# Kernel optimization log

Hardware: AMD Instinct MI355X
Metric: run time of the kernel (lower is better)

Reference implementation:

```python
import jax, jax.numpy as jnp
import numpy as np

EPS = 1e-5

def _ln(x, g, b):
    m = jnp.mean(x, axis=-1, keepdims=True)
    v = jnp.var(x, axis=-1, keepdims=True)
    return (x - m) / jnp.sqrt(v + EPS) * g + b

def setup_inputs() -> dict:
    key = jax.random.key(0)
    ks = jax.random.split(key, 16)
    B, T, N, K, d, E = 2, 12, 512, 8, 64, 64
    D = K * d
    s = 0.02
    inp = {
        "x": jax.random.normal(ks[0], (B, T, N, D), jnp.float32),
        "lapmatrix": jax.random.normal(ks[1], (N, N), jnp.float32),
        "node_embeddings": jax.random.normal(ks[2], (N, E), jnp.float32),
        "Wq": jax.random.normal(ks[3], (D, D), jnp.float32) * s,
        "bq": jnp.zeros((D,), jnp.float32),
        "Wk": jax.random.normal(ks[4], (D, D), jnp.float32) * s,
        "bk": jnp.zeros((D,), jnp.float32),
        "Wv": jax.random.normal(ks[5], (D, D), jnp.float32) * s,
        "bv": jnp.zeros((D,), jnp.float32),
        "Wo": jax.random.normal(ks[6], (D, D), jnp.float32) * s,
        "bo": jnp.zeros((D,), jnp.float32),
        "W1": jax.random.normal(ks[7], (4 * D, D), jnp.float32) * s,
        "b1": jnp.zeros((4 * D,), jnp.float32),
        "W2": jax.random.normal(ks[8], (D, 4 * D), jnp.float32) * s,
        "b2": jnp.zeros((D,), jnp.float32),
        "g1": jnp.ones((D,), jnp.float32),
        "be1": jnp.zeros((D,), jnp.float32),
        "g2": jnp.ones((D,), jnp.float32),
        "be2": jnp.zeros((D,), jnp.float32),
        "alpha": jnp.float32(1.0),
        "beta": jnp.float32(1.0),
        "k": 3,
    }
    return inp

def reference(x, lapmatrix, node_embeddings, Wq, bq, Wk, bk, Wv, bv, Wo, bo,
              W1, b1, W2, b2, g1, be1, g2, be2, alpha, beta, k):
    B, T, N, D = x.shape
    K, d = 8, D // 8
    x_raw = x
    xn = _ln(x, g1, be1)
    q = (xn @ Wq.T + bq).reshape(B, T, N, K, d)
    kk = (xn @ Wk.T + bk).reshape(B, T, N, K, d)
    v = (xn @ Wv.T + bv).reshape(B, T, N, K, d)
    # raw attention logits: [B,T,K,N,N]
    raw = jnp.einsum('btnkd,btmkd->btknm', q, kk) / jnp.sqrt(jnp.float32(d))
    # graph biases, all [N,N], broadcast over B,T,K
    supports = jax.nn.softmax(jax.nn.relu(node_embeddings @ node_embeddings.T), axis=1)
    adj = (lapmatrix != 0).astype(x.dtype)
    mask = jnp.where(adj == 0, jnp.float32(-1e9), jnp.float32(0.0))
    logits = raw + alpha * supports + beta * lapmatrix + mask
    attn = jax.nn.softmax(logits, axis=-1)  # dropout = identity in eval
    out = jnp.einsum('btknm,btmkd->btnkd', attn, v).reshape(B, T, N, D)
    x1 = x_raw + (out @ Wo.T + bo)
    h = _ln(x1, g2, be2)
    ffn = jax.nn.relu(h @ W1.T + b1) @ W2.T + b2
    return x1 + ffn
```

## Files before the change

### kernel.cpp

```cpp
#include <hip/hip_runtime.h>

typedef unsigned short u16;
typedef unsigned int   u32;
typedef __attribute__((ext_vector_type(8))) short bf16x8;
typedef __attribute__((ext_vector_type(4))) float f32x4;

#define DEV static __device__ __forceinline__

DEV float b2f(u16 u){ return __uint_as_float(((u32)u)<<16); }
DEV u16 f2b(float f){
  u32 u = __float_as_uint(f);
  u32 r = (u + 0x7FFFu + ((u>>16)&1u)) >> 16;
  return (u16)r;
}

union V8 { uint4 v; u16 s[8]; };

DEV u32 cvt_pk_bf16(float lo, float hi){
  u32 r;
  asm("v_cvt_pk_bf16_f32 %0, %1, %2" : "=v"(r) : "v"(lo), "v"(hi));
  return r;
}

DEV bool is_f32(const void* dt){ return *(const u32*)dt == 0x3F800000u; }

DEV uint4 ld8_ext_bf(const void* p, size_t i, bool f32){
  if(f32){
    const float* q = (const float*)p + i;
    float4 a = *(const float4*)q, b = *(const float4*)(q+4);
    V8 r;
    r.s[0]=f2b(a.x); r.s[1]=f2b(a.y); r.s[2]=f2b(a.z); r.s[3]=f2b(a.w);
    r.s[4]=f2b(b.x); r.s[5]=f2b(b.y); r.s[6]=f2b(b.z); r.s[7]=f2b(b.w);
    return r.v;
  }
  return *(const uint4*)((const u16*)p + i);
}
DEV void ld8_ext_f(const void* p, size_t i, bool f32, float* o){
  if(f32){
    const float* q = (const float*)p + i;
    float4 a = *(const float4*)q, b = *(const float4*)(q+4);
    o[0]=a.x;o[1]=a.y;o[2]=a.z;o[3]=a.w;o[4]=b.x;o[5]=b.y;o[6]=b.z;o[7]=b.w;
  }else{
    V8 u; u.v = *(const uint4*)((const u16*)p + i);
    #pragma unroll
    for(int k=0;k<8;k++) o[k]=b2f(u.s[k]);
  }
}
DEV float ld1_ext(const void* p, size_t i, bool f32){
  return f32 ? ((const float*)p)[i] : b2f(((const u16*)p)[i]);
}
DEV float load_scalar(const void* p, bool f32){
  return f32 ? *(const float*)p : b2f(*(const u16*)p);
}

DEV void gl_lds16(const u16* g, u16* l){
  __builtin_amdgcn_global_load_lds((const __attribute__((address_space(1))) void*)g,
                                   (__attribute__((address_space(3))) void*)l, 16, 0, 0);
}

__global__ __launch_bounds__(256) void sentinel_kernel(u16* out, long n, const void* dt){
  long ne = is_f32(dt) ? 2*n : n;
  long i = (long)blockIdx.x*256 + threadIdx.x;
  if(i < ne) out[i] = 0x4442;
}

__global__ __launch_bounds__(256) void prep_kernel(
    const void* __restrict__ x, const void* __restrict__ g1,
    const void* __restrict__ be1, u16* __restrict__ xn,
    const void* Wq, const void* Wk, const void* Wv, const void* Wo,
    const void* W1, const void* W2, u16* __restrict__ wbf,
    const void* bq, const void* bk, const void* bv, const void* bo,
    const void* b1, const void* b2, float* __restrict__ bfp,
    const void* __restrict__ E, const void* __restrict__ lap,
    const void* __restrict__ alpha_p, const void* __restrict__ beta_p,
    float* __restrict__ bm, const void* dt)
{
  __shared__ float En[64];
  __shared__ float red[8];
  const bool f32 = is_f32(dt);
  const int bid = blockIdx.x, t = threadIdx.x;

  if(bid < 3072){
    const int row = bid*4 + (t>>6), lane = t&63;
    float v[8];
    ld8_ext_f(x, (size_t)row*512 + lane*8, f32, v);
    float s=0.f, ss=0.f;
    #pragma unroll
    for(int i=0;i<8;i++){ s+=v[i]; ss+=v[i]*v[i]; }
    #pragma unroll
    for(int o=1;o<64;o<<=1){ s+=__shfl_xor(s,o,64); ss+=__shfl_xor(ss,o,64); }
    const float mean = s*(1.0f/512.0f);
    const float var  = ss*(1.0f/512.0f) - mean*mean;
    const float rstd = rsqrtf(var + 1e-5f);
    float gv[8], bv[8];
    ld8_ext_f(g1, (size_t)lane*8, f32, gv);
    ld8_ext_f(be1, (size_t)lane*8, f32, bv);
    V8 o8;
    #pragma unroll
    for(int i=0;i<8;i++) o8.s[i]=f2b((v[i]-mean)*rstd*gv[i]+bv[i]);
    *(uint4*)(xn+(size_t)row*512+lane*8)=o8.v;
  } else if(bid < 4608){
    size_t i = ((size_t)(bid-3072)*256 + t)*8;
    const void* src; size_t base;
    if(i < 262144){ src=Wq; base=0; }
    else if(i < 524288){ src=Wk; base=262144; }
    else if(i < 786432){ src=Wv; base=524288; }
    else if(i < 1048576){ src=Wo; base=786432; }
    else if(i < 2097152){ src=W1; base=1048576; }
    else { src=W2; base=2097152; }
    *(uint4*)(wbf + i) = ld8_ext_bf(src, i-base, f32);
  } else if(bid < 5120){
    const int n = bid - 4608;
    if(t < 64) En[t] = ld1_ext(E, (size_t)n*64 + t, f32);
    __syncthreads();
    const float alpha = load_scalar(alpha_p, f32);
    const float beta  = load_scalar(beta_p, f32);
    const int m0 = t, m1 = t+256;
    float sc0=0.f, sc1=0.f;
    #pragma unroll
    for(int c=0;c<8;c++){
      float a0[8], a1[8];
      ld8_ext_f(E, (size_t)m0*64 + c*8, f32, a0);
      ld8_ext_f(E, (size_t)m1*64 + c*8, f32, a1);
      #pragma unroll
      for(int j=0;j<8;j++){ const float en = En[c*8+j]; sc0 += en*a0[j]; sc1 += en*a1[j]; }
    }
    sc0 = fmaxf(sc0, 0.f); sc1 = fmaxf(sc1, 0.f);
    float mx = fmaxf(sc0, sc1);
    for(int o=1;o<64;o<<=1) mx = fmaxf(mx, __shfl_xor(mx,o,64));
    const int wave = t>>6;
    if((t&63)==0) red[wave]=mx;
    __syncthreads();
    mx = fmaxf(fmaxf(red[0],red[1]), fmaxf(red[2],red[3]));
    float e0 = __expf(sc0-mx), e1 = __expf(sc1-mx);
    float sm = e0+e1;
    for(int o=1;o<64;o<<=1) sm += __shfl_xor(sm,o,64);
    if((t&63)==0) red[4+wave]=sm;
    __syncthreads();
    sm = red[4]+red[5]+red[6]+red[7];
    const float inv = 1.f/sm;
    const int q0b = n>>5, iq = (n>>4)&1, l16 = n&15;
    const size_t qpart = (size_t)q0b*256 + (size_t)l16*4 + iq;
    float lv0 = ld1_ext(lap, (size_t)n*512+m0, f32);
    {
      float val = alpha*e0*inv + beta*lv0 + (lv0==0.f ? -1e9f : 0.f);
      int kb = m0>>3, e = m0&7;
      bm[(size_t)kb*4096 + qpart + (e>>1)*64 + (e&1)*2] = val;
    }
    float lv1 = ld1_ext(lap, (size_t)n*512+m1, f32);
    {
      float val = alpha*e1*inv + beta*lv1 + (lv1==0.f ? -1e9f : 0.f);
      int kb = m1>>3, e = m1&7;
      bm[(size_t)kb*4096 + qpart + (e>>1)*64 + (e&1)*2] = val;
    }
  } else {
    int j = (bid-5120)*256 + t;
    const void* src; int off;
    if(j < 512){ src=bq; off=0; }
    else if(j < 1024){ src=bk; off=512; }
    else if(j < 1536){ src=bv; off=1024; }
    else if(j < 2048){ src=bo; off=1536; }
    else if(j < 4096){ src=b1; off=2048; }
    else { src=b2; off=4096; }
    bfp[j] = ld1_ext(src, j-off, f32);
  }
}

template<int EXTIN>
__global__ __launch_bounds__(64) void ln_kernel(const void* __restrict__ xin,
    const void* __restrict__ g, const void* __restrict__ b, u16* __restrict__ out,
    const void* dt)
{
  const bool f32 = is_f32(dt);
  const int row = blockIdx.x, lane = threadIdx.x;
  float v[8];
  if(EXTIN){
    ld8_ext_f(xin, (size_t)row*512 + lane*8, f32, v);
  }else{
    V8 u; u.v = *(const uint4*)((const u16*)xin + (size_t)row*512 + lane*8);
    #pragma unroll
    for(int i=0;i<8;i++) v[i]=b2f(u.s[i]);
  }
  float s=0.f, ss=0.f;
  #pragma unroll
  for(int i=0;i<8;i++){ s+=v[i]; ss+=v[i]*v[i]; }
  #pragma unroll
  for(int o=1;o<64;o<<=1){ s+=__shfl_xor(s,o,64); ss+=__shfl_xor(ss,o,64); }
  const float mean = s*(1.0f/512.0f);
  const float var  = ss*(1.0f/512.0f) - mean*mean;
  const float rstd = rsqrtf(var + 1e-5f);
  float gv[8], bv[8];
  ld8_ext_f(g, (size_t)lane*8, f32, gv);
  ld8_ext_f(b, (size_t)lane*8, f32, bv);
  V8 o8;
  #pragma unroll
  for(int i=0;i<8;i++) o8.s[i]=f2b((v[i]-mean)*rstd*gv[i]+bv[i]);
  *(uint4*)(out+(size_t)row*512+lane*8)=o8.v;
}

template<int RELU, int RES, int RESEXT, int OUTEXT>
__global__ __launch_bounds__(256) void gemm_nt(
    const u16* __restrict__ A, const u16* __restrict__ B,
    const float* __restrict__ bias, const void* __restrict__ resid,
    void* __restrict__ Cout, int N, int K, const void* dt)
{
  __shared__ u16 As[2][128*32];
  __shared__ u16 Bs[2][128*32];
  const bool f32 = is_f32(dt);
  const int t = threadIdx.x;
  const int wave = t>>6, lane = t&63;
  const int n0 = blockIdx.y*128, m0 = blockIdx.x*128;
  const int wr = wave>>1, wc = wave&1;

  f32x4 acc[4][4];
  #pragma unroll
  for(int i=0;i<4;i++)
    #pragma unroll
    for(int j=0;j<4;j++){ acc[i][j][0]=0.f; acc[i][j][1]=0.f; acc[i][j][2]=0.f; acc[i][j][3]=0.f; }

  const int lrow16 = lane>>2, lg = lane&3;
  const int pgsw = (lg ^ ((lrow16>>1)&3))*8;
  const u16* Ag = A + (size_t)(m0+lrow16)*K + pgsw;
  const u16* Bg = B + (size_t)(n0+lrow16)*K + pgsw;

  const int fr = lane&15, qd = lane>>4;
  const int slot = (qd ^ ((fr>>1)&3))*8;
  const int aoff = (wr*64+fr)*32 + slot;
  const int boff = (wc*64+fr)*32 + slot;

  const int nt = K>>5;
  #pragma unroll
  for(int ii=0;ii<2;ii++){
    const int c = wave*2+ii;
    gl_lds16(Ag + (size_t)(c*16)*K, &As[0][c*512]);
    gl_lds16(Bg + (size_t)(c*16)*K, &Bs[0][c*512]);
  }
  __syncthreads();

  for(int tk=0; tk<nt; ++tk){
    const int cur = tk&1;
    if(tk+1 < nt){
      const int k0 = (tk+1)*32;
      #pragma unroll
      for(int ii=0;ii<2;ii++){
        const int c = wave*2+ii;
        gl_lds16(Ag + (size_t)(c*16)*K + k0, &As[cur^1][c*512]);
        gl_lds16(Bg + (size_t)(c*16)*K + k0, &Bs[cur^1][c*512]);
      }
    }
    const u16* Ab = As[cur];
    const u16* Bb = Bs[cur];
    bf16x8 af[4], bfr[4];
    #pragma unroll
    for(int i=0;i<4;i++) af[i] = *(const bf16x8*)&Ab[aoff + i*512];
    #pragma unroll
    for(int j=0;j<4;j++) bfr[j] = *(const bf16x8*)&Bb[boff + j*512];
    __builtin_amdgcn_s_setprio(1);
    #pragma unroll
    for(int i=0;i<4;i++)
      #pragma unroll
      for(int j=0;j<4;j++)
        acc[i][j] = __builtin_amdgcn_mfma_f32_16x16x32_bf16(af[i], bfr[j], acc[i][j], 0,0,0);
    __builtin_amdgcn_s_setprio(0);
    __syncthreads();
  }

  const int col16 = lane&15, rbase = (lane>>4)*4;
  #pragma unroll
  for(int i=0;i<4;i++){
    #pragma unroll
    for(int j=0;j<4;j++){
      const int gc = n0 + wc*64 + j*16 + col16;
      const float bv = bias[gc];
      #pragma unroll
      for(int r=0;r<4;r++){
        const int gr = m0 + wr*64 + i*16 + rbase + r;
        float val = acc[i][j][r] + bv;
        if(RELU) val = fmaxf(val, 0.f);
        if(RES){
          if(RESEXT) val += ld1_ext(resid, (size_t)gr*N+gc, f32);
          else       val += b2f(((const u16*)resid)[(size_t)gr*N+gc]);
        }
        if(OUTEXT && f32) ((float*)Cout)[(size_t)gr*N+gc] = val;
        else              ((u16*)Cout)[(size_t)gr*N+gc] = f2b(val);
      }
    }
  }
}

template<int RELU, int RES, int RESEXT, int OUTEXT>
__global__ __launch_bounds__(256) void gemm_nt64(
    const u16* __restrict__ A, const u16* __restrict__ B,
    const float* __restrict__ bias, const void* __restrict__ resid,
    void* __restrict__ Cout, int N, int K, const void* dt)
{
  __shared__ u16 As[2][128*32];
  __shared__ u16 Bs[2][64*32];
  const bool f32 = is_f32(dt);
  const int t = threadIdx.x;
  const int wave = t>>6, lane = t&63;
  const int n0 = blockIdx.y*64, m0 = blockIdx.x*128;
  const int wr = wave>>1, wc = wave&1;

  f32x4 acc[4][2];
  #pragma unroll
  for(int i=0;i<4;i++)
    #pragma unroll
    for(int j=0;j<2;j++){ acc[i][j][0]=0.f; acc[i][j][1]=0.f; acc[i][j][2]=0.f; acc[i][j][3]=0.f; }

  const int lrow16 = lane>>2, lg = lane&3;
  const int pgsw = (lg ^ ((lrow16>>1)&3))*8;
  const u16* Ag = A + (size_t)(m0+lrow16)*K + pgsw;
  const u16* Bg = B + (size_t)(n0+lrow16)*K + pgsw;

  const int fr = lane&15, qd = lane>>4;
  const int slot = (qd ^ ((fr>>1)&3))*8;
  const int aoff = (wr*64+fr)*32 + slot;
  const int boff = (wc*32+fr)*32 + slot;

  const int nt = K>>5;
  #pragma unroll
  for(int ii=0;ii<2;ii++){
    const int c = wave*2+ii;
    gl_lds16(Ag + (size_t)(c*16)*K, &As[0][c*512]);
  }
  gl_lds16(Bg + (size_t)(wave*16)*K, &Bs[0][wave*512]);
  __syncthreads();

  for(int tk=0; tk<nt; ++tk){
    const int cur = tk&1;
    if(tk+1 < nt){
      const int k0 = (tk+1)*32;
      #pragma unroll
      for(int ii=0;ii<2;ii++){
        const int c = wave*2+ii;
        gl_lds16(Ag + (size_t)(c*16)*K + k0, &As[cur^1][c*512]);
      }
      gl_lds16(Bg + (size_t)(wave*16)*K + k0, &Bs[cur^1][wave*512]);
    }
    const u16* Ab = As[cur];
    const u16* Bb = Bs[cur];
    bf16x8 af[4], bfr[2];
    #pragma unroll
    for(int i=0;i<4;i++) af[i] = *(const bf16x8*)&Ab[aoff + i*512];
    #pragma unroll
    for(int j=0;j<2;j++) bfr[j] = *(const bf16x8*)&Bb[boff + j*512];
    __builtin_amdgcn_s_setprio(1);
    #pragma unroll
    for(int i=0;i<4;i++)
      #pragma unroll
      for(int j=0;j<2;j++)
        acc[i][j] = __builtin_amdgcn_mfma_f32_16x16x32_bf16(af[i], bfr[j], acc[i][j], 0,0,0);
    __builtin_amdgcn_s_setprio(0);
    __syncthreads();
  }

  const int col16 = lane&15, rbase = (lane>>4)*4;
  #pragma unroll
  for(int i=0;i<4;i++){
    #pragma unroll
    for(int j=0;j<2;j++){
      const int gc = n0 + wc*32 + j*16 + col16;
      const float bv = bias[gc];
      #pragma unroll
      for(int r=0;r<4;r++){
        const int gr = m0 + wr*64 + i*16 + rbase + r;
        float val = acc[i][j][r] + bv;
        if(RELU) val = fmaxf(val, 0.f);
        if(RES){
          if(RESEXT) val += ld1_ext(resid, (size_t)gr*N+gc, f32);
          else       val += b2f(((const u16*)resid)[(size_t)gr*N+gc]);
        }
        if(OUTEXT && f32) ((float*)Cout)[(size_t)gr*N+gc] = val;
        else              ((u16*)Cout)[(size_t)gr*N+gc] = f2b(val);
      }
    }
  }
}

__global__ __launch_bounds__(256,3) void attn_kernel(
    const u16* __restrict__ qkv, const float* __restrict__ bm,
    u16* __restrict__ out)
{
  __shared__ u16 Kb[128*64];
  __shared__ u16 Vt[2][64*136];

  const int QS = 1536;
  const int t = threadIdx.x, wave = t>>6, lane = t&63;
  const int head = blockIdx.x, bt = blockIdx.z;
  const int q0 = blockIdx.y*128 + wave*32;
  const u16* qp = qkv + (size_t)bt*512*QS + head*64;
  const u16* kp = qp + 512;
  const u16* vp = qp + 1024;

  const int l16 = lane&15, qd = lane>>4;

  const int lrow8 = lane>>3, lg = lane&7;
  const int srow = t & 127;
  const int shalf = (t >> 7) * 32;
  const u16* vcp = vp + (size_t)srow*QS + shalf;

  #pragma unroll
  for(int ii=0;ii<4;ii++){
    const int c8 = wave*4 + ii;
    const int pg = lg ^ ((2*(lrow8&3) + (c8&3)) & 7);
    gl_lds16(kp + (size_t)(c8*8 + lrow8)*QS + pg*8, &Kb[c8*512]);
  }
  uint4 vv[4];
  #pragma unroll
  for(int qi=0;qi<4;qi++) vv[qi] = *(const uint4*)(vcp + qi*8);

  bf16x8 qf[2][2];
  #pragma unroll
  for(int i=0;i<2;i++)
    #pragma unroll
    for(int kc=0;kc<2;kc++)
      qf[i][kc] = *(const bf16x8*)(qp + (size_t)(q0 + i*16 + l16)*QS + kc*32 + qd*8);

  const float* bml = bm + (size_t)(blockIdx.y*4 + wave)*256 + (size_t)qd*4096 + (size_t)l16*4;

  const int arow = ((l16>>2)<<3) + (l16&3);
  const int rperm = (2*(l16&3) + (l16>>2)) & 7;
  const int g0 = (qd ^ rperm)*8;
  const u16* KA0 = &Kb[arow*64 + g0];
  const u16* KA1 = &Kb[arow*64 + (g0 ^ 32)];

  float mrun[2], lrun[2];
  mrun[0] = -3e38f; mrun[1] = -3e38f;
  lrun[0] = 0.f;    lrun[1] = 0.f;
  f32x4 oacc[2][4];
  #pragma unroll
  for(int i=0;i<2;i++)
    #pragma unroll
    for(int j=0;j<4;j++){ oacc[i][j][0]=0.f; oacc[i][j][1]=0.f; oacc[i][j][2]=0.f; oacc[i][j][3]=0.f; }

  #pragma unroll
  for(int qi=0;qi<4;qi++){
    V8 u; u.v = vv[qi];
    #pragma unroll
    for(int jj=0;jj<8;jj++) Vt[0][(shalf + qi*8 + jj)*136 + srow] = u.s[jj];
  }
  __syncthreads();

  #pragma unroll
  for(int c=0;c<4;c++){
    f32x4 p[2][8];
    __builtin_amdgcn_s_setprio(1);
    #pragma unroll
    for(int tt=0;tt<8;tt++){
      const int ro = (tt&3)*2048 + (tt>>2)*256;
      bf16x8 a0 = *(const bf16x8*)(KA0 + ro);
      bf16x8 a1 = *(const bf16x8*)(KA1 + ro);
      #pragma unroll
      for(int i=0;i<2;i++){
        f32x4 s; s[0]=0.f; s[1]=0.f; s[2]=0.f; s[3]=0.f;
        s = __builtin_amdgcn_mfma_f32_16x16x32_bf16(a0, qf[i][0], s, 0,0,0);
        s = __builtin_amdgcn_mfma_f32_16x16x32_bf16(a1, qf[i][1], s, 0,0,0);
        p[i][tt] = s;
      }
    }
    __builtin_amdgcn_s_setprio(0);
    if(c<3){
      __syncthreads();
      #pragma unroll
      for(int ii=0;ii<4;ii++){
        const int c8 = wave*4 + ii;
        const int pg = lg ^ ((2*(lrow8&3) + (c8&3)) & 7);
        gl_lds16(kp + (size_t)((c+1)*128 + c8*8 + lrow8)*QS + pg*8, &Kb[c8*512]);
      }
      #pragma unroll
      for(int qi=0;qi<4;qi++) vv[qi] = *(const uint4*)(vcp + (size_t)((c+1)*128)*QS + qi*8);
    }

    float mx0 = -3e38f, mx1 = -3e38f;
    #pragma unroll
    for(int s4=0;s4<4;s4++){
      const float* bp = bml + c*65536 + s4*16384;
      const float4 bg0 = *(const float4*)(bp);
      const float4 bg1 = *(const float4*)(bp + 64);
      const float4 bg2 = *(const float4*)(bp + 128);
      const float4 bg3 = *(const float4*)(bp + 192);
      #pragma unroll
      for(int i=0;i<2;i++){
        f32x4& pl = p[i][s4];
        pl[0] = pl[0]*0.125f + (i ? bg0.y : bg0.x);
        pl[1] = pl[1]*0.125f + (i ? bg0.w : bg0.z);
        pl[2] = pl[2]*0.125f + (i ? bg1.y : bg1.x);
        pl[3] = pl[3]*0.125f + (i ? bg1.w : bg1.z);
        f32x4& ph = p[i][s4+4];
        ph[0] = ph[0]*0.125f + (i ? bg2.y : bg2.x);
        ph[1] = ph[1]*0.125f + (i ? bg2.w : bg2.z);
        ph[2] = ph[2]*0.125f + (i ? bg3.y : bg3.x);
        ph[3] = ph[3]*0.125f + (i ? bg3.w : bg3.z);
        const float m8 = fmaxf(fmaxf(fmaxf(pl[0],pl[1]),fmaxf(pl[2],pl[3])),
                               fmaxf(fmaxf(ph[0],ph[1]),fmaxf(ph[2],ph[3])));
        if(i==0) mx0 = fmaxf(mx0, m8); else mx1 = fmaxf(mx1, m8);
      }
    }

    #pragma unroll
    for(int i=0;i<2;i++){
      float mx = i ? mx1 : mx0;
      mx = fmaxf(mx, __shfl_xor(mx, 16, 64));
      mx = fmaxf(mx, __shfl_xor(mx, 32, 64));
      const float mnew = fmaxf(mrun[i], mx);
      if(__any(mx > mrun[i])){
        const float al = __expf(mrun[i] - mnew);
        lrun[i] *= al;
        #pragma unroll
        for(int r=0;r<4;r++){
          const float alr = __shfl(al, (qd<<2)+r, 64);
          #pragma unroll
          for(int j=0;j<4;j++) oacc[i][j][r] *= alr;
        }
      }
      mrun[i] = mnew;
      float rs = 0.f;
      #pragma unroll
      for(int tt=0;tt<8;tt++){
        p[i][tt][0] = __expf(p[i][tt][0]-mnew);
        p[i][tt][1] = __expf(p[i][tt][1]-mnew);
        p[i][tt][2] = __expf(p[i][tt][2]-mnew);
        p[i][tt][3] = __expf(p[i][tt][3]-mnew);
        rs += (p[i][tt][0]+p[i][tt][1]) + (p[i][tt][2]+p[i][tt][3]);
      }
      rs += __shfl_xor(rs, 16, 64);
      rs += __shfl_xor(rs, 32, 64);
      lrun[i] += rs;
    }

    __builtin_amdgcn_s_setprio(1);
    #pragma unroll
    for(int ks=0;ks<4;ks++){
      union { bf16x8 v; u32 w[4]; } pa[2];
      #pragma unroll
      for(int i=0;i<2;i++){
        pa[i].w[0] = cvt_pk_bf16(p[i][ks][0],   p[i][ks][1]);
        pa[i].w[1] = cvt_pk_bf16(p[i][ks][2],   p[i][ks][3]);
        pa[i].w[2] = cvt_pk_bf16(p[i][ks+4][0], p[i][ks+4][1]);
        pa[i].w[3] = cvt_pk_bf16(p[i][ks+4][2], p[i][ks+4][3]);
      }
      #pragma unroll
      for(int j=0;j<4;j++){
        bf16x8 bvf = *(const bf16x8*)&Vt[c&1][(j*16 + l16)*136 + ks*32 + qd*8];
        oacc[0][j] = __builtin_amdgcn_mfma_f32_16x16x32_bf16(pa[0].v, bvf, oacc[0][j], 0,0,0);
        oacc[1][j] = __builtin_amdgcn_mfma_f32_16x16x32_bf16(pa[1].v, bvf, oacc[1][j], 0,0,0);
      }
    }
    __builtin_amdgcn_s_setprio(0);

    if(c<3){
      #pragma unroll
      for(int qi=0;qi<4;qi++){
        V8 u; u.v = vv[qi];
        #pragma unroll
        for(int jj=0;jj<8;jj++) Vt[(c+1)&1][(shalf + qi*8 + jj)*136 + srow] = u.s[jj];
      }
      __syncthreads();
    }
  }

  u16* op = out + (size_t)bt*512*512 + head*64;
  #pragma unroll
  for(int i=0;i<2;i++){
    const float inv = 1.f / lrun[i];
    #pragma unroll
    for(int r=0;r<4;r++){
      const float invr = __shfl(inv, (qd<<2)+r, 64);
      const size_t rowb = (size_t)(q0 + i*16 + qd*4 + r)*512;
      #pragma unroll
      for(int j=0;j<4;j++)
        op[rowb + j*16 + l16] = f2b(oacc[i][j][r] * invr);
    }
  }
}

extern "C" void kernel_launch(void* const* d_in, const int* in_sizes, int n_in,
                              void* d_out, int out_size, void* d_ws, size_t ws_size,
                              hipStream_t stream) {
  const void* x   = d_in[0];
  const void* lap = d_in[1];
  const void* ne  = d_in[2];
  const void* Wq  = d_in[3];
  const void* bq  = d_in[4];
  const void* Wk  = d_in[5];
  const void* bk  = d_in[6];
  const void* Wv  = d_in[7];
  const void* bv  = d_in[8];
  const void* Wo  = d_in[9];
  const void* bo  = d_in[10];
  const void* W1  = d_in[11];
  const void* b1  = d_in[12];
  const void* W2  = d_in[13];
  const void* b2  = d_in[14];
  const void* g1  = d_in[15];
  const void* be1 = d_in[16];
  const void* g2  = d_in[17];
  const void* be2 = d_in[18];
  const void* alpha = d_in[19];
  const void* beta  = d_in[20];
  const void* dt = g1;

  const int M = 12288;
  const size_t NEED = (size_t)512*512*4 + (size_t)M*512*2*2 + (size_t)M*2048*2
                    + (size_t)3145728*2 + (size_t)4608*4;
  if(ws_size < NEED){
    long n = out_size;
    sentinel_kernel<<<(2*n+255)/256, 256, 0, stream>>>((u16*)d_out, n, dt);
    return;
  }
  char* w = (char*)d_ws;
  float* bias_m = (float*)w;              w += (size_t)512*512*4;
  u16*   slotB  = (u16*)w;                w += (size_t)M*512*2;
  char*  slotC  = w;                      w += (size_t)M*2048*2;
  u16*   x1     = (u16*)w;                w += (size_t)M*512*2;
  u16*   wbf    = (u16*)w;                w += (size_t)3145728*2;
  float* bfp    = (float*)w;
  u16* qkv = (u16*)slotC;
  u16* h1  = (u16*)slotC;
  u16* xn = slotB;
  u16* ao = slotB;
  u16* h  = slotB;

  prep_kernel<<<5138, 256, 0, stream>>>(
      x, g1, be1, xn,
      Wq, Wk, Wv, Wo, W1, W2, wbf,
      bq, bk, bv, bo, b1, b2, bfp,
      ne, lap, alpha, beta, bias_m, dt);
  gemm_nt<0,0,0,0><<<dim3(96,12), 256, 0, stream>>>(xn, wbf, bfp, nullptr, qkv, 1536, 512, dt);
  attn_kernel<<<dim3(8,4,24), 256, 0, stream>>>(qkv, bias_m, ao);
  gemm_nt64<0,1,1,0><<<dim3(96,8), 256, 0, stream>>>(ao, wbf+786432, bfp+1536, x, x1, 512, 512, dt);
  ln_kernel<0><<<M, 64, 0, stream>>>(x1, g2, be2, h, dt);
  gemm_nt<1,0,0,0><<<dim3(96,16), 256, 0, stream>>>(h, wbf+1048576, bfp+2048, nullptr, h1, 2048, 512, dt);
  gemm_nt64<0,1,0,1><<<dim3(96,8), 256, 0, stream>>>(h1, wbf+2097152, bfp+4096, x1, d_out, 512, 2048, dt);
}
```

Before: 336.0 us.

## Deepen GEMM LDS pipelines to triple/quad buffering with explicit vmcnt waits

Both bf16 GEMM kernels switch from double-buffered LDS staging with a full __syncthreads per k-tile to a 3-stage (128x128) and 4-stage (128x64) ring of global_load_lds buffers. Partial s_waitcnt vmcnt waits plus a single raw s_barrier per iteration keep more loads in flight and drop the trailing barrier. The aim is to hide global memory latency behind MFMA work. In exchange, LDS use grows (48KB and 48KB per block), which can lower occupancy, and correctness depends on the hand-counted vmcnt values.

```diff
diff --git a/kernel.cpp b/kernel.cpp
--- a/kernel.cpp
+++ b/kernel.cpp
@@ -57,6 +57,13 @@
   __builtin_amdgcn_global_load_lds((const __attribute__((address_space(1))) void*)g,
                                    (__attribute__((address_space(3))) void*)l, 16, 0, 0);
 }
+
+#define WAITV(n) asm volatile("s_waitcnt vmcnt(" #n ")" ::: "memory")
+#define PIPE_BARRIER() do { \
+  __builtin_amdgcn_sched_barrier(0); \
+  __builtin_amdgcn_s_barrier(); \
+  __builtin_amdgcn_sched_barrier(0); \
+} while(0)
 
 __global__ __launch_bounds__(256) void sentinel_kernel(u16* out, long n, const void* dt){
   long ne = is_f32(dt) ? 2*n : n;
@@ -204,8 +211,8 @@
     const float* __restrict__ bias, const void* __restrict__ resid,
     void* __restrict__ Cout, int N, int K, const void* dt)
 {
-  __shared__ u16 As[2][128*32];
-  __shared__ u16 Bs[2][128*32];
+  __shared__ u16 As[3][128*32];
+  __shared__ u16 Bs[3][128*32];
   const bool f32 = is_f32(dt);
   const int t = threadIdx.x;
   const int wave = t>>6, lane = t&63;
@@ -228,28 +235,29 @@
   const int aoff = (wr*64+fr)*32 + slot;
   const int boff = (wc*64+fr)*32 + slot;
 
+  const int c0 = wave*2, c1 = wave*2+1;
+  #define STAGE_G(tt, bb) do { \
+    const int k0s = (tt)*32; \
+    gl_lds16(Ag + (size_t)(c0*16)*K + k0s, &As[bb][c0*512]); \
+    gl_lds16(Ag + (size_t)(c1*16)*K + k0s, &As[bb][c1*512]); \
+    gl_lds16(Bg + (size_t)(c0*16)*K + k0s, &Bs[bb][c0*512]); \
+    gl_lds16(Bg + (size_t)(c1*16)*K + k0s, &Bs[bb][c1*512]); \
+  } while(0)
+
   const int nt = K>>5;
-  #pragma unroll
-  for(int ii=0;ii<2;ii++){
-    const int c = wave*2+ii;
-    gl_lds16(Ag + (size_t)(c*16)*K, &As[0][c*512]);
-    gl_lds16(Bg + (size_t)(c*16)*K, &Bs[0][c*512]);
-  }
-  __syncthreads();
-
+  STAGE_G(0,0);
+  STAGE_G(1,1);
+  int buf = 0;
   for(int tk=0; tk<nt; ++tk){
-    const int cur = tk&1;
-    if(tk+1 < nt){
-      const int k0 = (tk+1)*32;
-      #pragma unroll
-      for(int ii=0;ii<2;ii++){
-        const int c = wave*2+ii;
-        gl_lds16(Ag + (size_t)(c*16)*K + k0, &As[cur^1][c*512]);
-        gl_lds16(Bg + (size_t)(c*16)*K + k0, &Bs[cur^1][c*512]);
-      }
-    }
-    const u16* Ab = As[cur];
-    const u16* Bb = Bs[cur];
+    if(tk < nt-1) WAITV(4);
+    else          WAITV(0);
+    PIPE_BARRIER();
+    if(tk+2 < nt){
+      int nb = buf+2; if(nb>=3) nb-=3;
+      STAGE_G(tk+2, nb);
+    }
+    const u16* Ab = As[buf];
+    const u16* Bb = Bs[buf];
     bf16x8 af[4], bfr[4];
     #pragma unroll
     for(int i=0;i<4;i++) af[i] = *(const bf16x8*)&Ab[aoff + i*512];
@@ -262,8 +270,9 @@
       for(int j=0;j<4;j++)
         acc[i][j] = __builtin_amdgcn_mfma_f32_16x16x32_bf16(af[i], bfr[j], acc[i][j], 0,0,0);
     __builtin_amdgcn_s_setprio(0);
-    __syncthreads();
-  }
+    buf = (buf+1==3) ? 0 : buf+1;
+  }
+  #undef STAGE_G
 
   const int col16 = lane&15, rbase = (lane>>4)*4;
   #pragma unroll
@@ -294,8 +303,8 @@
     const float* __restrict__ bias, const void* __restrict__ resid,
     void* __restrict__ Cout, int N, int K, const void* dt)
 {
-  __shared__ u16 As[2][128*32];
-  __shared__ u16 Bs[2][64*32];
+  __shared__ u16 As[4][128*32];
+  __shared__ u16 Bs[4][64*32];
   const bool f32 = is_f32(dt);
   const int t = threadIdx.x;
   const int wave = t>>6, lane = t&63;
@@ -318,28 +327,29 @@
   const int aoff = (wr*64+fr)*32 + slot;
   const int boff = (wc*32+fr)*32 + slot;
 
+  const int c0 = wave*2, c1 = wave*2+1;
+  #define STAGE_G64(tt, bb) do { \
+    const int k0s = (tt)*32; \
+    gl_lds16(Ag + (size_t)(c0*16)*K + k0s, &As[bb][c0*512]); \
+    gl_lds16(Ag + (size_t)(c1*16)*K + k0s, &As[bb][c1*512]); \
+    gl_lds16(Bg + (size_t)(wave*16)*K + k0s, &Bs[bb][wave*512]); \
+  } while(0)
+
   const int nt = K>>5;
-  #pragma unroll
-  for(int ii=0;ii<2;ii++){
-    const int c = wave*2+ii;
-    gl_lds16(Ag + (size_t)(c*16)*K, &As[0][c*512]);
-  }
-  gl_lds16(Bg + (size_t)(wave*16)*K, &Bs[0][wave*512]);
-  __syncthreads();
-
+  STAGE_G64(0,0);
+  STAGE_G64(1,1);
+  STAGE_G64(2,2);
   for(int tk=0; tk<nt; ++tk){
-    const int cur = tk&1;
-    if(tk+1 < nt){
-      const int k0 = (tk+1)*32;
-      #pragma unroll
-      for(int ii=0;ii<2;ii++){
-        const int c = wave*2+ii;
-        gl_lds16(Ag + (size_t)(c*16)*K + k0, &As[cur^1][c*512]);
-      }
-      gl_lds16(Bg + (size_t)(wave*16)*K + k0, &Bs[cur^1][wave*512]);
-    }
-    const u16* Ab = As[cur];
-    const u16* Bb = Bs[cur];
+    if(tk < nt-2)      WAITV(6);
+    else if(tk == nt-2) WAITV(3);
+    else               WAITV(0);
+    PIPE_BARRIER();
+    if(tk+3 < nt){
+      STAGE_G64(tk+3, (tk+3)&3);
+    }
+    const int buf = tk&3;
+    const u16* Ab = As[buf];
+    const u16* Bb = Bs[buf];
     bf16x8 af[4], bfr[2];
     #pragma unroll
     for(int i=0;i<4;i++) af[i] = *(const bf16x8*)&Ab[aoff + i*512];
@@ -352,8 +362,8 @@
       for(int j=0;j<2;j++)
         acc[i][j] = __builtin_amdgcn_mfma_f32_16x16x32_bf16(af[i], bfr[j], acc[i][j], 0,0,0);
     __builtin_amdgcn_s_setprio(0);
-    __syncthreads();
-  }
+  }
+  #undef STAGE_G64
 
   const int col16 = lane&15, rbase = (lane>>4)*4;
   #pragma unroll
```

New measurement: 332.9 us. About the same (-0.9%).
